# Kernel optimization log

Measured on AMD Instinct MI355X. Metric: run time of the kernel, lower is better.

The kernel has to match this reference:

```python
import jax, jax.numpy as jnp
import numpy as np

UP = 2
NUM_POINT = 9
GROUPS = 4


def pixel_shuffle(t, r):
    # [B, C*r*r, H, W] -> [B, C, H*r, W*r], torch layout: in[b, c*r*r + i*r + j, h, w] -> out[b, c, h*r+i, w*r+j]
    B, C, H, W = t.shape
    Co = C // (r * r)
    t = t.reshape(B, Co, r, r, H, W)
    t = t.transpose(0, 1, 4, 2, 5, 3)
    return t.reshape(B, Co, H * r, W * r)


def _bilinear_sample(feat, py, px):
    # feat: [E, H, W]; py, px: [P, Hup, Wup] in low-res pixel coords (zero padding outside)
    H, W = feat.shape[1], feat.shape[2]
    y0f = jnp.floor(py)
    x0f = jnp.floor(px)
    ty = py - y0f
    tx = px - x0f
    y0 = y0f.astype(jnp.int32)
    x0 = x0f.astype(jnp.int32)
    out = jnp.zeros(feat.shape[:1] + py.shape, dtype=feat.dtype)
    corners = ((0, 0, (1 - ty) * (1 - tx)), (0, 1, (1 - ty) * tx),
               (1, 0, ty * (1 - tx)), (1, 1, ty * tx))
    for dy, dx, w in corners:
        yi = y0 + dy
        xi = x0 + dx
        valid = ((yi >= 0) & (yi < H) & (xi >= 0) & (xi < W)).astype(feat.dtype)
        yc = jnp.clip(yi, 0, H - 1)
        xc = jnp.clip(xi, 0, W - 1)
        out = out + feat[:, yc, xc] * (w * valid)[None]
    return out  # [E, P, Hup, Wup]

# vmap over batch and group dims
_sample_bg = jax.vmap(jax.vmap(_bilinear_sample))


def setup_inputs() -> dict:
    key = jax.random.key(0)
    ks = jax.random.split(key, 8)
    B, Cy, Cx = 2, 256, 256
    H, W = 64, 64
    Hup, Wup = H * UP, W * UP
    GE = GROUPS * 32              # q/k channels = groups * embedding_dim
    OFF = GROUPS * NUM_POINT * 2 * UP * UP  # 288
    return {
        "y": jax.random.normal(ks[0], (B, Cy, Hup, Wup), jnp.float32),
        "x": jax.random.normal(ks[1], (B, Cx, H, W), jnp.float32),
        "Wq": jax.random.normal(ks[2], (GE, Cy), jnp.float32) * 0.02,
        "bq": jnp.zeros((GE,), jnp.float32),
        "Wk": jax.random.normal(ks[3], (GE, Cx), jnp.float32) * 0.02,
        "bk": jnp.zeros((GE,), jnp.float32),
        "Woff": jax.random.normal(ks[4], (OFF, Cx), jnp.float32) * 0.02,
        "boff": jnp.zeros((OFF,), jnp.float32),
    }


def reference(y, x, Wq, bq, Wk, bk, Woff, boff):
    G, P, up = GROUPS, NUM_POINT, UP
    B, C, H, W = x.shape
    # 1x1 convs as einsum
    q = jnp.einsum('oi,bihw->bohw', Wq, y) + bq[None, :, None, None]
    k = jnp.einsum('oi,bihw->bohw', Wk, x) + bk[None, :, None, None]
    off = jnp.einsum('oi,bihw->bohw', Woff, x) + boff[None, :, None, None]
    off = pixel_shuffle(off, up)  # [B, G*P*2, Hup, Wup]
    Hup, Wup = off.shape[2], off.shape[3]
    off = off.reshape(B, G, P, 2, Hup, Wup)
    # sampling positions in low-res coordinates: align-centers base + learned offset
    base_y = (jnp.arange(Hup, dtype=jnp.float32) + 0.5) / up - 0.5
    base_x = (jnp.arange(Wup, dtype=jnp.float32) + 0.5) / up - 0.5
    py = off[:, :, :, 0] + base_y[None, None, None, :, None]  # [B,G,P,Hup,Wup]
    px = off[:, :, :, 1] + base_x[None, None, None, None, :]
    E = Wq.shape[0] // G
    qg = q.reshape(B, G, E, Hup, Wup)
    kg = k.reshape(B, G, E, H, W)
    # deform_qk: gather k at offset points, dot with q over embedding dim
    ks = _sample_bg(kg, py, px)                    # [B,G,E,P,Hup,Wup]
    attn = jnp.einsum('bgehw,bgephw->bgphw', qg, ks)
    attn = jax.nn.softmax(attn, axis=2)            # softmax over points
    # deform_av: gather x at the same points, weighted sum by attn
    Cg = C // G
    xg = x.reshape(B, G, Cg, H, W)
    xs = _sample_bg(xg, py, px)                    # [B,G,Cg,P,Hup,Wup]
    out = jnp.einsum('bgphw,bgcphw->bgchw', attn, xs)
    return out.reshape(B, C, Hup, Wup)
```

## Files before the change

### kernel.cpp

```cpp
#include <hip/hip_runtime.h>

#define B_N   2
#define H_LR  64
#define W_LR  64
#define HUP   128
#define WUP   128
#define GRP   4
#define NPT   9
#define EMB   32
#define CGRP  64
#define KIN   256
#define GE    128
#define NOFF  288

typedef __attribute__((ext_vector_type(8))) short short8v;
typedef _Float16 half8v __attribute__((ext_vector_type(8)));
typedef __attribute__((ext_vector_type(4))) float f32x4;

__device__ __forceinline__ ushort f2bf(float f) {
    unsigned u = __float_as_uint(f);
    u += 0x7FFFu + ((u >> 16) & 1u);
    return (ushort)(u >> 16);
}
__device__ __forceinline__ float bf2f(ushort h) {
    return __uint_as_float(((unsigned)h) << 16);
}
__device__ __forceinline__ ushort f2h(float f) {
    _Float16 h = (_Float16)f;
    return __builtin_bit_cast(ushort, h);
}
__device__ __forceinline__ float h2f(ushort u) {
    _Float16 h = __builtin_bit_cast(_Float16, u);
    return (float)h;
}

__global__ __launch_bounds__(256, 4) void mfma_gemm(
    const float* __restrict__ y, const float* __restrict__ x,
    const float* __restrict__ Wq, const float* __restrict__ Wk,
    const float* __restrict__ Woff,
    const float* __restrict__ bq, const float* __restrict__ bk,
    const float* __restrict__ boff,
    ushort* __restrict__ qbf, ushort* __restrict__ kbf,
    ushort* __restrict__ offh)
{
    __shared__ __align__(16) ushort sY[64][68];
    __shared__ __align__(16) ushort sB[128][72];

    int bid = blockIdx.x;
    const float* SRC; const float* ba; const float* bb;
    ushort* OBF; ushort* OFH;
    int M, m0, n0, b;
    bool isQ = (bid < 512);
    if (isQ) {
        int mt = bid & 255; b = bid >> 8;
        SRC = y; ba = bq; bb = nullptr; OBF = qbf; OFH = nullptr;
        M = 16384; m0 = mt * 64; n0 = 0;
    } else {
        int r = bid - 512;
        int mt = r & 63, nt2 = (r >> 6) & 3; b = r >> 8;
        SRC = x; ba = bk; bb = boff; OBF = kbf; OFH = offh;
        M = 4096; m0 = mt * 64; n0 = nt2 * 128;
    }

    int tid = threadIdx.x;
    int lane = tid & 63;
    int wv = tid >> 6, wm = wv >> 1, wn = wv & 1;
    int il = lane & 15, g4 = lane >> 4;
    int st_m4 = tid & 15, st_c = tid >> 4;
    int st_c8 = tid & 7,  st_n = tid >> 3;

    const float* wrowp[4];
#pragma unroll
    for (int i = 0; i < 4; ++i) {
        int n = n0 + st_n + i * 32;
        if (isQ)            wrowp[i] = Wq  + (size_t)n * KIN;
        else if (n < GE)    wrowp[i] = Wk  + (size_t)n * KIN;
        else if (n < GE + NOFF) wrowp[i] = Woff + (size_t)(n - GE) * KIN;
        else                wrowp[i] = nullptr;
    }

    f32x4 acc[2][4];
#pragma unroll
    for (int i = 0; i < 2; ++i)
#pragma unroll
        for (int j = 0; j < 4; ++j) { f32x4 z = {0.f,0.f,0.f,0.f}; acc[i][j] = z; }

    const float* src_b = SRC + (size_t)b * KIN * M;

    float4 ra[4]; short8v rb[4];
#pragma unroll
    for (int i = 0; i < 4; ++i)
        ra[i] = *(const float4*)&src_b[(size_t)(st_c + i * 16) * M + m0 + st_m4 * 4];
#pragma unroll
    for (int i = 0; i < 4; ++i) {
        short8v t = {0,0,0,0,0,0,0,0};
        if (wrowp[i]) {
            float4 a = *(const float4*)&wrowp[i][st_c8 * 8];
            float4 c = *(const float4*)&wrowp[i][st_c8 * 8 + 4];
            t[0]=(short)f2bf(a.x); t[1]=(short)f2bf(a.y); t[2]=(short)f2bf(a.z); t[3]=(short)f2bf(a.w);
            t[4]=(short)f2bf(c.x); t[5]=(short)f2bf(c.y); t[6]=(short)f2bf(c.z); t[7]=(short)f2bf(c.w);
        }
        rb[i] = t;
    }

    for (int ks = 0; ks < 4; ++ks) {
#pragma unroll
        for (int i = 0; i < 4; ++i) {
            ushort4 h;
            h.x = f2bf(ra[i].x); h.y = f2bf(ra[i].y);
            h.z = f2bf(ra[i].z); h.w = f2bf(ra[i].w);
            *(ushort4*)&sY[st_c + i * 16][st_m4 * 4] = h;
            *(short8v*)&sB[st_n + i * 32][st_c8 * 8] = rb[i];
        }
        __syncthreads();
        if (ks < 3) {
            int k0 = (ks + 1) * 64;
#pragma unroll
            for (int i = 0; i < 4; ++i)
                ra[i] = *(const float4*)&src_b[(size_t)(k0 + st_c + i * 16) * M + m0 + st_m4 * 4];
#pragma unroll
            for (int i = 0; i < 4; ++i) {
                short8v t = {0,0,0,0,0,0,0,0};
                if (wrowp[i]) {
                    float4 a = *(const float4*)&wrowp[i][k0 + st_c8 * 8];
                    float4 c = *(const float4*)&wrowp[i][k0 + st_c8 * 8 + 4];
                    t[0]=(short)f2bf(a.x); t[1]=(short)f2bf(a.y); t[2]=(short)f2bf(a.z); t[3]=(short)f2bf(a.w);
                    t[4]=(short)f2bf(c.x); t[5]=(short)f2bf(c.y); t[6]=(short)f2bf(c.z); t[7]=(short)f2bf(c.w);
                }
                rb[i] = t;
            }
        }
#pragma unroll
        for (int kc = 0; kc < 2; ++kc) {
            int kb = kc * 32 + g4 * 8;
            short8v af[2], bfr[4];
#pragma unroll
            for (int mf = 0; mf < 2; ++mf) {
                int m = wm * 32 + mf * 16 + il;
                short8v t;
#pragma unroll
                for (int j = 0; j < 8; ++j) t[j] = (short)sY[kb + j][m];
                af[mf] = t;
            }
#pragma unroll
            for (int nf = 0; nf < 4; ++nf)
                bfr[nf] = *(const short8v*)&sB[wn * 64 + nf * 16 + il][kb];
#pragma unroll
            for (int mf = 0; mf < 2; ++mf)
#pragma unroll
                for (int nf = 0; nf < 4; ++nf)
                    acc[mf][nf] = __builtin_amdgcn_mfma_f32_16x16x32_bf16(
                        af[mf], bfr[nf], acc[mf][nf], 0, 0, 0);
        }
        __syncthreads();
    }

#pragma unroll
    for (int mf = 0; mf < 2; ++mf) {
#pragma unroll
        for (int r = 0; r < 4; ++r) {
            int m = m0 + wm * 32 + mf * 16 + g4 * 4 + r;
            size_t row = (size_t)b * M + m;
#pragma unroll
            for (int nf = 0; nf < 4; ++nf) {
                int n = n0 + wn * 64 + nf * 16 + il;
                float v = acc[mf][nf][r];
                if (n < GE) {
                    OBF[row * 128 + n] = f2bf(v + ba[n]);
                } else {
                    int no = n - GE;
                    if (no < NOFF) OFH[row * 288 + no] = f2h(v + bb[no]);
                }
            }
        }
    }
}

#define RROWS 6
#define RCOLS 11
#define RPX   66

__global__ __launch_bounds__(256, 4) void deform_kernel(
    const ushort* __restrict__ qbf,
    const ushort* __restrict__ kbf,
    const ushort* __restrict__ offh,
    const float* __restrict__ x,
    float* __restrict__ out)
{
    __shared__ __align__(16) ushort sXt[64][72];
    __shared__ __align__(16) ushort sK[66][40];
    __shared__ __align__(16) ushort sQ[64][40];
    __shared__ __align__(16) ushort sSW[64][72];
    __shared__ uint   sGt[576];
    __shared__ int    sGz[576];
    __shared__ __align__(16) float sAttn[576];
    __shared__ int    sFB[129];

    int bxl = blockIdx.x;
    int bx = (bxl & 7) * 256 + (bxl >> 3);
    int tw = bx & 7, th = (bx >> 3) & 31, g = (bx >> 8) & 3, b = bx >> 10;
    int tid = threadIdx.x;
    int wv_ = tid >> 6, lane = tid & 63;
    int row = lane & 15, kb8 = lane >> 4;

    const int ry0 = th * 2 - 2, rx0 = tw * 8 - 1;
    ushort* sOffA = (ushort*)sAttn;

    if (tid == 0) sFB[0] = 0;
    for (int s = tid; s < 384; s += 256) {
        int gy = s % 6, ch = s / 6;
        int gyg = min(max(ry0 + gy, 0), 63);
        const float* xr = x + ((size_t)b * 256 + g * CGRP + ch) * 4096 + gyg * 64;
        float v[11];
        if (tw >= 1 && tw <= 6) {
            int a0 = rx0 - 3;
            float tmp[16];
#pragma unroll
            for (int t4 = 0; t4 < 4; ++t4) {
                float4 f = *(const float4*)&xr[a0 + t4 * 4];
                tmp[t4*4+0] = f.x; tmp[t4*4+1] = f.y; tmp[t4*4+2] = f.z; tmp[t4*4+3] = f.w;
            }
#pragma unroll
            for (int qx = 0; qx < RCOLS; ++qx) v[qx] = tmp[qx + 3];
        } else {
#pragma unroll
            for (int qx = 0; qx < RCOLS; ++qx) {
                int gxg = min(max(rx0 + qx, 0), 63);
                v[qx] = xr[gxg];
            }
        }
        ushort* dst = &sXt[ch][0];
        int c0 = gy * RCOLS;
        if (c0 & 1) {
            dst[c0] = f2h(v[0]);
#pragma unroll
            for (int j = 0; j < 5; ++j)
                *(uint*)&dst[c0 + 1 + 2*j] =
                    (uint)f2h(v[1 + 2*j]) | ((uint)f2h(v[2 + 2*j]) << 16);
        } else {
#pragma unroll
            for (int j = 0; j < 5; ++j)
                *(uint*)&dst[c0 + 2*j] =
                    (uint)f2h(v[2*j]) | ((uint)f2h(v[1 + 2*j]) << 16);
            dst[c0 + 10] = f2h(v[10]);
        }
    }
    for (int i = tid; i < 264; i += 256) {
        int rp = i >> 2, c4 = i & 3;
        int qy = rp / RCOLS, qx = rp - qy * RCOLS;
        int gy = min(max(ry0 + qy, 0), 63), gx = min(max(rx0 + qx, 0), 63);
        *(short8v*)&sK[rp][c4 * 8] =
            *(const short8v*)&kbf[((size_t)b * 4096 + gy * 64 + gx) * 128 +
                                  g * EMB + c4 * 8];
    }
    {
        int px = tid >> 2, c4 = tid & 3;
        int hup = th * 4 + (px >> 4), wup = tw * 16 + (px & 15);
        *(short8v*)&sQ[px][c4 * 8] =
            *(const short8v*)&qbf[((size_t)b * 16384 + hup * 128 + wup) * 128 +
                                  g * EMB + c4 * 8];
    }
    for (int i = tid; i < 144; i += 256) {
        int lr = i / 9, f8 = i - (i / 9) * 9;
        int yy = th * 2 + (lr >> 3), xx = tw * 8 + (lr & 7);
        *(short8v*)&sOffA[lr * 72 + f8 * 8] =
            *(const short8v*)&offh[((size_t)b * 4096 + yy * 64 + xx) * 288 +
                                   g * 72 + f8 * 8];
    }
    __syncthreads();

    {
        short8v a = *(const short8v*)&sQ[wv_ * 16 + row][kb8 * 8];
#pragma unroll
        for (int nt = 0; nt < 5; ++nt) {
            int rr = nt * 16 + row; if (rr > 65) rr = 65;
            short8v bf = *(const short8v*)&sK[rr][kb8 * 8];
            f32x4 z = {0.f, 0.f, 0.f, 0.f};
            f32x4 d = __builtin_amdgcn_mfma_f32_16x16x32_bf16(a, bf, z, 0, 0, 0);
            int rp = nt * 16 + row;
            if (rp < RPX) {
#pragma unroll
                for (int r = 0; r < 4; ++r)
                    sSW[wv_ * 16 + kb8 * 4 + r][rp] = f2h(d[r]);
            }
        }
    }
    for (int item = tid; item < 576; item += 256) {
        int px = item / 9, pt = item - (item / 9) * 9;
        int lx = px & 15, ly = px >> 4;
        int hup = th * 4 + ly, wup = tw * 16 + lx;
        int lr = (ly >> 1) * 8 + (lx >> 1);
        int ij = ((hup & 1) << 1) | (wup & 1);
        float offy = h2f(sOffA[lr * 72 + pt * 8 + ij]);
        float offx = h2f(sOffA[lr * 72 + pt * 8 + 4 + ij]);
        float py  = offy + hup * 0.5f - 0.25f;
        float pxx = offx + wup * 0.5f - 0.25f;
        float y0f = floorf(py), x0f = floorf(pxx);
        float ty = py - y0f, tx = pxx - x0f;
        int y0 = (int)y0f, x0 = (int)x0f;
        int mk = 0;
        if ((unsigned)y0 < 64u && (unsigned)x0 < 64u)         mk |= 1;
        if ((unsigned)y0 < 64u && (unsigned)(x0+1) < 64u)     mk |= 2;
        if ((unsigned)(y0+1) < 64u && (unsigned)x0 < 64u)     mk |= 4;
        if ((unsigned)(y0+1) < 64u && (unsigned)(x0+1) < 64u) mk |= 8;
        int iy = y0 - ry0, ix = x0 - rx0;
        bool inreg = ((unsigned)iy <= (unsigned)(RROWS - 2)) &&
                     ((unsigned)ix <= (unsigned)(RCOLS - 2));
        int fl, zp;
        if (!mk)        { fl = 16; zp = 0; }
        else if (inreg) { fl = mk | 16; zp = iy * RCOLS + ix; }
        else            { fl = mk; zp = (y0 + 1) * 66 + (x0 + 1); }
        sGt[item] = (uint)f2h(ty) | ((uint)f2h(tx) << 16);
        sGz[item] = (zp << 5) | fl;
    }
    __syncthreads();

    for (int item = tid; item < 576; item += 256) {
        int px = item / 9;
        uint gt = sGt[item];
        float ty = h2f((ushort)gt), tx = h2f((ushort)(gt >> 16));
        int z = sGz[item];
        int fl = z & 31;
        float a;
        if (fl & 16) {
            int zi = z >> 5;
            float w00 = (1.f - ty) * (1.f - tx), w01 = (1.f - ty) * tx;
            float w10 = ty * (1.f - tx), w11 = ty * tx;
            a  = (fl & 1) ? w00 * h2f(sSW[px][zi])             : 0.f;
            a += (fl & 2) ? w01 * h2f(sSW[px][zi + 1])         : 0.f;
            a += (fl & 4) ? w10 * h2f(sSW[px][zi + RCOLS])     : 0.f;
            a += (fl & 8) ? w11 * h2f(sSW[px][zi + RCOLS + 1]) : 0.f;
        } else {
            int t = z >> 5;
            int y0 = t / 66 - 1, x0 = t - (t / 66) * 66 - 1;
            a = 0.f;
#pragma unroll
            for (int c = 0; c < 4; ++c) if ((fl >> c) & 1) {
                int dy = c >> 1, dx = c & 1;
                float wgt = (dy ? ty : 1.f - ty) * (dx ? tx : 1.f - tx);
                const ushort* kr = &kbf[((size_t)b * 4096 + (y0 + dy) * 64 + x0 + dx) * 128 +
                                        g * EMB];
                float dot = 0.f;
                for (int e = 0; e < EMB; ++e) dot += bf2f(sQ[px][e]) * bf2f(kr[e]);
                a += wgt * dot;
            }
            int old = atomicAdd(&sFB[0], 1);
            if (old < 128) sFB[1 + old] = item;
        }
        sAttn[item] = a;
    }
    __syncthreads();

    if (tid < 64) {
        int px = tid;
        float aa[NPT];
        float mx = -1e30f;
#pragma unroll
        for (int p = 0; p < NPT; ++p) { aa[p] = sAttn[px * 9 + p]; mx = fmaxf(mx, aa[p]); }
        float s = 0.f;
#pragma unroll
        for (int p = 0; p < NPT; ++p) { aa[p] = __expf(aa[p] - mx); s += aa[p]; }
        float inv = 1.f / s;
#pragma unroll
        for (int p = 0; p < NPT; ++p) { aa[p] *= inv; sAttn[px * 9 + p] = aa[p]; }
        {
            float4 z4 = make_float4(0.f, 0.f, 0.f, 0.f);
            char* wr = (char*)&sSW[px][0];
#pragma unroll
            for (int j = 0; j < 9; ++j) *(float4*)(wr + j * 16) = z4;
        }
#pragma unroll
        for (int pt = 0; pt < NPT; ++pt) {
            int item = px * 9 + pt;
            int z = sGz[item];
            int fl = z & 31;
            if (!(fl & 16)) continue;
            uint gt = sGt[item];
            float ty = h2f((ushort)gt), tx = h2f((ushort)(gt >> 16));
            float a = aa[pt];
            int zi = z >> 5;
            ushort* c = &sSW[px][zi];
            if (fl & 1) c[0]         = f2h(h2f(c[0])         + (1.f-ty)*(1.f-tx)*a);
            if (fl & 2) c[1]         = f2h(h2f(c[1])         + (1.f-ty)*tx*a);
            if (fl & 4) c[RCOLS]     = f2h(h2f(c[RCOLS])     + ty*(1.f-tx)*a);
            if (fl & 8) c[RCOLS + 1] = f2h(h2f(c[RCOLS + 1]) + ty*tx*a);
        }
    }
    __syncthreads();

    {
        half8v bfm[2][4];
#pragma unroll
        for (int kt = 0; kt < 2; ++kt)
#pragma unroll
            for (int nt = 0; nt < 4; ++nt)
                bfm[kt][nt] = *(const half8v*)&sXt[nt * 16 + row][kt * 32 + kb8 * 8];

        int px = wv_ * 16 + row;
        half8v af0 = *(const half8v*)&sSW[px][kb8 * 8];
        half8v af1 = *(const half8v*)&sSW[px][32 + kb8 * 8];

        f32x4 acc[4];
#pragma unroll
        for (int nt = 0; nt < 4; ++nt) { f32x4 z = {0.f,0.f,0.f,0.f}; acc[nt] = z; }
#pragma unroll
        for (int nt = 0; nt < 4; ++nt) {
            acc[nt] = __builtin_amdgcn_mfma_f32_16x16x32_f16(af0, bfm[0][nt], acc[nt], 0, 0, 0);
            acc[nt] = __builtin_amdgcn_mfma_f32_16x16x32_f16(af1, bfm[1][nt], acc[nt], 0, 0, 0);
        }
        float wc[4][2];
#pragma unroll
        for (int r = 0; r < 4; ++r) {
            uint u = *(uint*)&sSW[wv_ * 16 + kb8 * 4 + r][64];
            wc[r][0] = h2f((ushort)u); wc[r][1] = h2f((ushort)(u >> 16));
        }
#pragma unroll
        for (int nt = 0; nt < 4; ++nt) {
            uint u = *(uint*)&sXt[nt * 16 + row][64];
            float x0 = h2f((ushort)u), x1 = h2f((ushort)(u >> 16));
#pragma unroll
            for (int r = 0; r < 4; ++r)
                acc[nt][r] += wc[r][0] * x0 + wc[r][1] * x1;
        }
        int hup = th * 4 + wv_;
#pragma unroll
        for (int nt = 0; nt < 4; ++nt) {
            int ch = nt * 16 + row;
            float* ob = out + ((size_t)b * 256 + g * CGRP + ch) * 16384 +
                        hup * 128 + tw * 16 + kb8 * 4;
#pragma unroll
            for (int r = 0; r < 4; ++r) ob[r] = acc[nt][r];
        }
    }

    int nfb = min(sFB[0], 128);
    if (nfb > 0) {
        __syncthreads();
        for (int i = 0; i < nfb; ++i) {
            if (tid < 64) {
                int item = sFB[1 + i];
                int px = item / 9;
                uint gt = sGt[item];
                float ty = h2f((ushort)gt), tx = h2f((ushort)(gt >> 16));
                int z = sGz[item];
                float a = sAttn[item];
                int fl = z & 15;
                int t = z >> 5;
                int y0 = t / 66 - 1, x0 = t - (t / 66) * 66 - 1;
                const float* xg = x + ((size_t)b * 256 + g * CGRP + tid) * 4096;
                float v = 0.f;
                if (fl & 1) v += (1.f-ty)*(1.f-tx)*a * xg[y0*64 + x0];
                if (fl & 2) v += (1.f-ty)*tx*a       * xg[y0*64 + x0 + 1];
                if (fl & 4) v += ty*(1.f-tx)*a       * xg[(y0+1)*64 + x0];
                if (fl & 8) v += ty*tx*a             * xg[(y0+1)*64 + x0 + 1];
                int hup = th * 4 + (px >> 4), wup = tw * 16 + (px & 15);
                float* op = out + ((size_t)b * 256 + g * CGRP + tid) * 16384 +
                            hup * 128 + wup;
                *op += v;
            }
        }
    }
}

extern "C" void kernel_launch(void* const* d_in, const int* in_sizes, int n_in,
                              void* d_out, int out_size, void* d_ws, size_t ws_size,
                              hipStream_t stream)
{
    const float* y    = (const float*)d_in[0];
    const float* x    = (const float*)d_in[1];
    const float* Wq   = (const float*)d_in[2];
    const float* bq   = (const float*)d_in[3];
    const float* Wk   = (const float*)d_in[4];
    const float* bk   = (const float*)d_in[5];
    const float* Woff = (const float*)d_in[6];
    const float* boff = (const float*)d_in[7];
    float* out = (float*)d_out;

    ushort* qbf   = (ushort*)d_ws;
    ushort* kbf   = qbf + (size_t)B_N * 16384 * 128;
    ushort* offh  = kbf + (size_t)B_N * 4096 * 128;

    mfma_gemm<<<dim3(1024), dim3(256), 0, stream>>>(
        y, x, Wq, Wk, Woff, bq, bk, boff, qbf, kbf, offh);

    deform_kernel<<<dim3(2048), dim3(256), 0, stream>>>(qbf, kbf, offh, x, out);
}
```

Before: 61.30 us.

## Make attention stages wave-local and replace block barriers with fences

Each wave now handles the 144 sampling items for its own 16 pixels. The geometry pass and the attention-logit pass are fused into one loop, and the offsets move into a dedicated shared buffer instead of aliasing sAttn. Several __syncthreads are replaced with __threadfence_block, so waves no longer wait on each other between the logit, softmax and weight-scatter stages. The weighted-value MFMA reads sXt rows written by other waves in the prologue, so correctness now depends on the earlier barrier. Adding a barrier before the fallback loop makes the block always synchronise at the end.

```diff
diff --git a/kernel.cpp b/kernel.cpp
--- a/kernel.cpp
+++ b/kernel.cpp
@@ -191,9 +191,10 @@
     __shared__ __align__(16) ushort sK[66][40];
     __shared__ __align__(16) ushort sQ[64][40];
     __shared__ __align__(16) ushort sSW[64][72];
+    __shared__ __align__(16) ushort sOffH[16 * 72];
     __shared__ uint   sGt[576];
     __shared__ int    sGz[576];
-    __shared__ __align__(16) float sAttn[576];
+    __shared__ float  sAttn[576];
     __shared__ int    sFB[129];
 
     int bxl = blockIdx.x;
@@ -204,7 +205,6 @@
     int row = lane & 15, kb8 = lane >> 4;
 
     const int ry0 = th * 2 - 2, rx0 = tw * 8 - 1;
-    ushort* sOffA = (ushort*)sAttn;
 
     if (tid == 0) sFB[0] = 0;
     for (int s = tid; s < 384; s += 256) {
@@ -263,7 +263,7 @@
     for (int i = tid; i < 144; i += 256) {
         int lr = i / 9, f8 = i - (i / 9) * 9;
         int yy = th * 2 + (lr >> 3), xx = tw * 8 + (lr & 7);
-        *(short8v*)&sOffA[lr * 72 + f8 * 8] =
+        *(short8v*)&sOffH[lr * 72 + f8 * 8] =
             *(const short8v*)&offh[((size_t)b * 4096 + yy * 64 + xx) * 288 +
                                    g * 72 + f8 * 8];
     }
@@ -285,74 +285,70 @@
             }
         }
     }
-    for (int item = tid; item < 576; item += 256) {
-        int px = item / 9, pt = item - (item / 9) * 9;
-        int lx = px & 15, ly = px >> 4;
-        int hup = th * 4 + ly, wup = tw * 16 + lx;
-        int lr = (ly >> 1) * 8 + (lx >> 1);
-        int ij = ((hup & 1) << 1) | (wup & 1);
-        float offy = h2f(sOffA[lr * 72 + pt * 8 + ij]);
-        float offx = h2f(sOffA[lr * 72 + pt * 8 + 4 + ij]);
-        float py  = offy + hup * 0.5f - 0.25f;
-        float pxx = offx + wup * 0.5f - 0.25f;
-        float y0f = floorf(py), x0f = floorf(pxx);
-        float ty = py - y0f, tx = pxx - x0f;
-        int y0 = (int)y0f, x0 = (int)x0f;
-        int mk = 0;
-        if ((unsigned)y0 < 64u && (unsigned)x0 < 64u)         mk |= 1;
-        if ((unsigned)y0 < 64u && (unsigned)(x0+1) < 64u)     mk |= 2;
-        if ((unsigned)(y0+1) < 64u && (unsigned)x0 < 64u)     mk |= 4;
-        if ((unsigned)(y0+1) < 64u && (unsigned)(x0+1) < 64u) mk |= 8;
-        int iy = y0 - ry0, ix = x0 - rx0;
-        bool inreg = ((unsigned)iy <= (unsigned)(RROWS - 2)) &&
-                     ((unsigned)ix <= (unsigned)(RCOLS - 2));
-        int fl, zp;
-        if (!mk)        { fl = 16; zp = 0; }
-        else if (inreg) { fl = mk | 16; zp = iy * RCOLS + ix; }
-        else            { fl = mk; zp = (y0 + 1) * 66 + (x0 + 1); }
-        sGt[item] = (uint)f2h(ty) | ((uint)f2h(tx) << 16);
-        sGz[item] = (zp << 5) | fl;
-    }
-    __syncthreads();
-
-    for (int item = tid; item < 576; item += 256) {
-        int px = item / 9;
-        uint gt = sGt[item];
-        float ty = h2f((ushort)gt), tx = h2f((ushort)(gt >> 16));
-        int z = sGz[item];
-        int fl = z & 31;
-        float a;
-        if (fl & 16) {
-            int zi = z >> 5;
-            float w00 = (1.f - ty) * (1.f - tx), w01 = (1.f - ty) * tx;
-            float w10 = ty * (1.f - tx), w11 = ty * tx;
-            a  = (fl & 1) ? w00 * h2f(sSW[px][zi])             : 0.f;
-            a += (fl & 2) ? w01 * h2f(sSW[px][zi + 1])         : 0.f;
-            a += (fl & 4) ? w10 * h2f(sSW[px][zi + RCOLS])     : 0.f;
-            a += (fl & 8) ? w11 * h2f(sSW[px][zi + RCOLS + 1]) : 0.f;
-        } else {
-            int t = z >> 5;
-            int y0 = t / 66 - 1, x0 = t - (t / 66) * 66 - 1;
-            a = 0.f;
-#pragma unroll
-            for (int c = 0; c < 4; ++c) if ((fl >> c) & 1) {
-                int dy = c >> 1, dx = c & 1;
-                float wgt = (dy ? ty : 1.f - ty) * (dx ? tx : 1.f - tx);
-                const ushort* kr = &kbf[((size_t)b * 4096 + (y0 + dy) * 64 + x0 + dx) * 128 +
-                                        g * EMB];
-                float dot = 0.f;
-                for (int e = 0; e < EMB; ++e) dot += bf2f(sQ[px][e]) * bf2f(kr[e]);
-                a += wgt * dot;
-            }
-            int old = atomicAdd(&sFB[0], 1);
-            if (old < 128) sFB[1 + old] = item;
-        }
-        sAttn[item] = a;
-    }
-    __syncthreads();
-
-    if (tid < 64) {
-        int px = tid;
+    __threadfence_block();
+
+    for (int it = 0; it < 3; ++it) {
+        int idx = it * 64 + lane;
+        if (idx < 144) {
+            int item = wv_ * 144 + idx;
+            int px = item / 9, pt = item - px * 9;
+            int lx = px & 15, ly = px >> 4;
+            int hup = th * 4 + ly, wup = tw * 16 + lx;
+            int lr = (ly >> 1) * 8 + (lx >> 1);
+            int ij = ((hup & 1) << 1) | (wup & 1);
+            float offy = h2f(sOffH[lr * 72 + pt * 8 + ij]);
+            float offx = h2f(sOffH[lr * 72 + pt * 8 + 4 + ij]);
+            float py  = offy + hup * 0.5f - 0.25f;
+            float pxx = offx + wup * 0.5f - 0.25f;
+            float y0f = floorf(py), x0f = floorf(pxx);
+            float ty = py - y0f, tx = pxx - x0f;
+            int y0 = (int)y0f, x0 = (int)x0f;
+            int mk = 0;
+            if ((unsigned)y0 < 64u && (unsigned)x0 < 64u)         mk |= 1;
+            if ((unsigned)y0 < 64u && (unsigned)(x0+1) < 64u)     mk |= 2;
+            if ((unsigned)(y0+1) < 64u && (unsigned)x0 < 64u)     mk |= 4;
+            if ((unsigned)(y0+1) < 64u && (unsigned)(x0+1) < 64u) mk |= 8;
+            int iy = y0 - ry0, ix = x0 - rx0;
+            bool inreg = ((unsigned)iy <= (unsigned)(RROWS - 2)) &&
+                         ((unsigned)ix <= (unsigned)(RCOLS - 2));
+            int fl, zp;
+            if (!mk)        { fl = 16; zp = 0; }
+            else if (inreg) { fl = mk | 16; zp = iy * RCOLS + ix; }
+            else            { fl = mk; zp = (y0 + 1) * 66 + (x0 + 1); }
+            sGt[item] = (uint)f2h(ty) | ((uint)f2h(tx) << 16);
+            sGz[item] = (zp << 5) | fl;
+
+            float a;
+            if (fl & 16) {
+                int zi = zp;
+                float w00 = (1.f - ty) * (1.f - tx), w01 = (1.f - ty) * tx;
+                float w10 = ty * (1.f - tx), w11 = ty * tx;
+                a  = (fl & 1) ? w00 * h2f(sSW[px][zi])             : 0.f;
+                a += (fl & 2) ? w01 * h2f(sSW[px][zi + 1])         : 0.f;
+                a += (fl & 4) ? w10 * h2f(sSW[px][zi + RCOLS])     : 0.f;
+                a += (fl & 8) ? w11 * h2f(sSW[px][zi + RCOLS + 1]) : 0.f;
+            } else {
+                a = 0.f;
+#pragma unroll
+                for (int c = 0; c < 4; ++c) if ((mk >> c) & 1) {
+                    int dy = c >> 1, dx = c & 1;
+                    float wgt = (dy ? ty : 1.f - ty) * (dx ? tx : 1.f - tx);
+                    const ushort* kr = &kbf[((size_t)b * 4096 + (y0 + dy) * 64 + x0 + dx) * 128 +
+                                            g * EMB];
+                    float dot = 0.f;
+                    for (int e = 0; e < EMB; ++e) dot += bf2f(sQ[px][e]) * bf2f(kr[e]);
+                    a += wgt * dot;
+                }
+                int old = atomicAdd(&sFB[0], 1);
+                if (old < 128) sFB[1 + old] = item;
+            }
+            sAttn[item] = a;
+        }
+    }
+    __threadfence_block();
+
+    if (lane < 16) {
+        int px = wv_ * 16 + lane;
         float aa[NPT];
         float mx = -1e30f;
 #pragma unroll
@@ -386,7 +382,7 @@
             if (fl & 8) c[RCOLS + 1] = f2h(h2f(c[RCOLS + 1]) + ty*tx*a);
         }
     }
-    __syncthreads();
+    __threadfence_block();
 
     {
         half8v bfm[2][4];
@@ -433,31 +429,29 @@
         }
     }
 
+    __syncthreads();
     int nfb = min(sFB[0], 128);
-    if (nfb > 0) {
-        __syncthreads();
-        for (int i = 0; i < nfb; ++i) {
-            if (tid < 64) {
-                int item = sFB[1 + i];
-                int px = item / 9;
-                uint gt = sGt[item];
-                float ty = h2f((ushort)gt), tx = h2f((ushort)(gt >> 16));
-                int z = sGz[item];
-                float a = sAttn[item];
-                int fl = z & 15;
-                int t = z >> 5;
-                int y0 = t / 66 - 1, x0 = t - (t / 66) * 66 - 1;
-                const float* xg = x + ((size_t)b * 256 + g * CGRP + tid) * 4096;
-                float v = 0.f;
-                if (fl & 1) v += (1.f-ty)*(1.f-tx)*a * xg[y0*64 + x0];
-                if (fl & 2) v += (1.f-ty)*tx*a       * xg[y0*64 + x0 + 1];
-                if (fl & 4) v += ty*(1.f-tx)*a       * xg[(y0+1)*64 + x0];
-                if (fl & 8) v += ty*tx*a             * xg[(y0+1)*64 + x0 + 1];
-                int hup = th * 4 + (px >> 4), wup = tw * 16 + (px & 15);
-                float* op = out + ((size_t)b * 256 + g * CGRP + tid) * 16384 +
-                            hup * 128 + wup;
-                *op += v;
-            }
+    for (int i = 0; i < nfb; ++i) {
+        if (tid < 64) {
+            int item = sFB[1 + i];
+            int px = item / 9;
+            uint gt = sGt[item];
+            float ty = h2f((ushort)gt), tx = h2f((ushort)(gt >> 16));
+            int z = sGz[item];
+            float a = sAttn[item];
+            int fl = z & 15;
+            int t = z >> 5;
+            int y0 = t / 66 - 1, x0 = t - (t / 66) * 66 - 1;
+            const float* xg = x + ((size_t)b * 256 + g * CGRP + tid) * 4096;
+            float v = 0.f;
+            if (fl & 1) v += (1.f-ty)*(1.f-tx)*a * xg[y0*64 + x0];
+            if (fl & 2) v += (1.f-ty)*tx*a       * xg[y0*64 + x0 + 1];
+            if (fl & 4) v += ty*(1.f-tx)*a       * xg[(y0+1)*64 + x0];
+            if (fl & 8) v += ty*tx*a             * xg[(y0+1)*64 + x0 + 1];
+            int hup = th * 4 + (px >> 4), wup = tw * 16 + (px & 15);
+            float* op = out + ((size_t)b * 256 + g * CGRP + tid) * 16384 +
+                        hup * 128 + wup;
+            *op += v;
         }
     }
 }
```

New measurement: 60.89 us (median of 2 runs). About the same (-0.7%).
